# Optimization experiments

Hardware: AMD Instinct MI355X
Metric: run time of the kernel (lower is better)

Reference implementation:

```python
import jax, jax.numpy as jnp
import numpy as np

EPS_LN = 1e-5
EPS_STD = 1e-5


def _ln_dim1(z, g, b):
    # LayerNorm over channel dim (axis=1) of (B, C, T) or (B, C, 1)
    mu = z.mean(axis=1, keepdims=True)
    var = ((z - mu) ** 2).mean(axis=1, keepdims=True)
    return (z - mu) * jax.lax.rsqrt(var + EPS_LN) * g[None, :, None] + b[None, :, None]


def _stats(x, m):
    # weighted mean/std over time axis; m broadcasts over channels
    mean = (m * x).sum(axis=2)                                   # (B, C)
    std = jnp.sqrt(jnp.maximum((m * x * x).sum(axis=2) - mean ** 2, EPS_STD))
    return mean, std


def setup_inputs() -> dict:
    key = jax.random.key(0)
    ks = jax.random.split(key, 4)
    B, C, T, H = 16, 1536, 2000, 128
    x = jax.random.normal(ks[0], (B, C, T), dtype=jnp.float32)
    mask = jnp.ones((B, 1, T), dtype=jnp.float32)
    # attention MLP params (conv1x1 -> relu -> LN(dim=1) -> tanh -> conv1x1)
    w1 = jax.random.normal(ks[1], (H, 3 * C), dtype=jnp.float32) * (1.0 / np.sqrt(3 * C))
    b1 = jnp.zeros((H,), jnp.float32)
    g1 = jnp.ones((H,), jnp.float32)
    be1 = jnp.zeros((H,), jnp.float32)
    w2 = jax.random.normal(ks[2], (C, H), dtype=jnp.float32) * (1.0 / np.sqrt(H))
    b2 = jnp.zeros((C,), jnp.float32)
    g2 = jnp.ones((2 * C,), jnp.float32)
    be2 = jnp.zeros((2 * C,), jnp.float32)
    return {"x": x, "mask": mask, "w1": w1, "b1": b1, "g1": g1, "be1": be1,
            "w2": w2, "b2": b2, "g2": g2, "be2": be2}


def reference(x, mask, w1, b1, g1, be1, w2, b2, g2, be2):
    B, C, T = x.shape
    # time_attention: append masked global mean/std, broadcast over T
    total = mask.sum(axis=2, keepdims=True)                      # (B,1,1)
    mean0, std0 = _stats(x, mask / total)                        # (B,C)
    x_in = jnp.concatenate([
        x,
        jnp.broadcast_to(mean0[:, :, None], (B, C, T)),
        jnp.broadcast_to(std0[:, :, None], (B, C, T)),
    ], axis=1)                                                   # (B,3C,T)
    # attention MLP (conv1x1 == channel matmul)
    h = jnp.einsum("hc,bct->bht", w1, x_in) + b1[None, :, None]  # (B,H,T)
    h = jnp.tanh(_ln_dim1(jax.nn.relu(h), g1, be1))
    alpha = jnp.einsum("ch,bht->bct", w2, h) + b2[None, :, None]  # (B,C,T)
    # masked softmax over time
    alpha = jnp.where(mask == 0, -jnp.inf, alpha)
    alpha = jax.nn.softmax(alpha, axis=2)
    # attention-weighted stats
    mean, std = _stats(x, alpha)                                 # (B,C) each
    out = jnp.concatenate([mean, std], axis=1)[:, :, None]       # (B,2C,1)
    return _ln_dim1(out, g2, be2)
```

## Files before the change

### kernel.cpp

```cpp
#include <hip/hip_runtime.h>
#include <hip/hip_bf16.h>
#include <math.h>

constexpr int B_  = 16;
constexpr int C_  = 1536;
constexpr int T_  = 2000;
constexpr int H_  = 128;
constexpr int C3_ = 3 * C_;
constexpr int C2_ = 2 * C_;
constexpr int NT_ = 4;
constexpr int NTL_ = 32;
constexpr int KH_ = C_ / 2;

typedef short bf8 __attribute__((ext_vector_type(8)));
typedef short bf4 __attribute__((ext_vector_type(4)));
typedef float f4  __attribute__((ext_vector_type(4)));

__device__ inline unsigned short f2b(float f) {
  __bf16 h = (__bf16)f;
  return __builtin_bit_cast(unsigned short, h);
}

__global__ __launch_bounds__(256) void k_gemm1_stats(
    const float* __restrict__ x, const float* __restrict__ w1,
    const float* __restrict__ mask,
    float* __restrict__ h_pre, float* __restrict__ sp1, float* __restrict__ sp2) {
  __shared__ __align__(16) short As[2][128 * 32];
  __shared__ __align__(16) short Bs[2][64 * 32];
  const int b = blockIdx.y;
  const int tile = blockIdx.x;
  const int kbase = blockIdx.z * KH_;
  const int t0 = tile * 64;
  const int tid = threadIdx.x;
  const int lane = tid & 63;
  const int w = tid >> 6;
  const int l15 = lane & 15;
  const int l4 = lane >> 4;

  float4 va[4], vb[2];

  const int t4 = tid & 15;
  float mreg[4];
#pragma unroll
  for (int j = 0; j < 4; ++j) {
    int t = t0 + t4 * 4 + j;
    mreg[j] = (t < T_) ? mask[(size_t)b * T_ + t] : 0.f;
  }
  float* sp1row = sp1 + ((size_t)b * NTL_ + tile) * C_;
  float* sp2row = sp2 + ((size_t)b * NTL_ + tile) * C_;

  f4 acc[8];
#pragma unroll
  for (int mi = 0; mi < 8; ++mi) { f4 z = {0.f, 0.f, 0.f, 0.f}; acc[mi] = z; }

#define G1_GLOAD(K0)                                                          \
  {                                                                           \
    _Pragma("unroll")                                                         \
    for (int q = 0; q < 4; ++q) {                                             \
      int idx = q * 256 + tid;                                                \
      int row = idx >> 3, j4 = idx & 7;                                       \
      va[q] = *(const float4*)(w1 + (size_t)row * C3_ + (K0) + j4 * 4);       \
    }                                                                         \
    _Pragma("unroll")                                                         \
    for (int q = 0; q < 2; ++q) {                                             \
      int idx = q * 256 + tid;                                                \
      int k = idx >> 4;                                                       \
      int t = t0 + t4 * 4;                                                    \
      if (t < T_)                                                             \
        vb[q] = *(const float4*)(x + ((size_t)(b * C_ + (K0) + k)) * T_ + t); \
      else                                                                    \
        vb[q] = make_float4(0.f, 0.f, 0.f, 0.f);                              \
    }                                                                         \
  }
#define G1_LSTORE(BUF)                                                        \
  {                                                                           \
    _Pragma("unroll")                                                         \
    for (int q = 0; q < 4; ++q) {                                             \
      int idx = q * 256 + tid;                                                \
      int row = idx >> 3, j4 = idx & 7;                                       \
      int slot = (j4 >> 1) ^ ((row >> 2) & 3);                                \
      bf4 p;                                                                  \
      p[0] = (short)f2b(va[q].x); p[1] = (short)f2b(va[q].y);                 \
      p[2] = (short)f2b(va[q].z); p[3] = (short)f2b(va[q].w);                 \
      *(bf4*)&As[BUF][row * 32 + slot * 8 + (j4 & 1) * 4] = p;                \
    }                                                                         \
    _Pragma("unroll")                                                         \
    for (int q = 0; q < 2; ++q) {                                             \
      int idx = q * 256 + tid;                                                \
      int k = idx >> 4;                                                       \
      float vv[4] = {vb[q].x, vb[q].y, vb[q].z, vb[q].w};                     \
      _Pragma("unroll")                                                       \
      for (int j = 0; j < 4; ++j) {                                           \
        int row = t4 * 4 + j;                                                 \
        int slot = (k >> 3) ^ ((row >> 2) & 3);                               \
        Bs[BUF][row * 32 + slot * 8 + (k & 7)] = (short)f2b(vv[j]);           \
      }                                                                       \
    }                                                                         \
  }
#define G1_STATS(K0)                                                          \
  {                                                                           \
    _Pragma("unroll")                                                         \
    for (int q = 0; q < 2; ++q) {                                             \
      float vv[4] = {vb[q].x, vb[q].y, vb[q].z, vb[q].w};                     \
      float a1 = 0.f, a2 = 0.f;                                               \
      _Pragma("unroll")                                                       \
      for (int j = 0; j < 4; ++j) {                                           \
        float mx = mreg[j] * vv[j];                                           \
        a1 += mx;                                                             \
        a2 = fmaf(mx, vv[j], a2);                                             \
      }                                                                       \
      _Pragma("unroll")                                                       \
      for (int off = 1; off < 16; off <<= 1) {                                \
        a1 += __shfl_xor(a1, off);                                            \
        a2 += __shfl_xor(a2, off);                                            \
      }                                                                       \
      if (t4 == 0) {                                                          \
        int c = (K0) + q * 16 + (tid >> 4);                                   \
        sp1row[c] = a1;                                                       \
        sp2row[c] = a2;                                                       \
      }                                                                       \
    }                                                                         \
  }

  G1_GLOAD(kbase);
  G1_LSTORE(0);
  G1_STATS(kbase);
  __syncthreads();

  const int fA = (l15 >> 2) & 3;
  const int NS = KH_ / 32;
  for (int s = 0; s < NS; ++s) {
    const int cur = s & 1;
    if (s + 1 < NS) G1_GLOAD(kbase + (s + 1) * 32);
    {
      const int browB = w * 16 + l15;
      bf8 bfr = *(const bf8*)&Bs[cur][browB * 32 + (l4 ^ fA) * 8];
#pragma unroll
      for (int mi = 0; mi < 8; ++mi) {
        bf8 afr = *(const bf8*)&As[cur][(mi * 16 + l15) * 32 + (l4 ^ fA) * 8];
        acc[mi] = __builtin_amdgcn_mfma_f32_16x16x32_bf16(afr, bfr, acc[mi], 0, 0, 0);
      }
    }
    if (s + 1 < NS) {
      G1_LSTORE(cur ^ 1);
      G1_STATS(kbase + (s + 1) * 32);
    }
    __syncthreads();
  }

  const int t = t0 + w * 16 + l15;
  if (t < T_) {
    float* dst = h_pre + (size_t)blockIdx.z * B_ * T_ * H_ + ((size_t)b * T_ + t) * H_;
#pragma unroll
    for (int mi = 0; mi < 8; ++mi)
      *(f4*)&dst[mi * 16 + l4 * 4] = acc[mi];
  }
}

__global__ __launch_bounds__(256) void k_stats_reduce(
    const float* __restrict__ sp1, const float* __restrict__ sp2,
    const float* __restrict__ mask,
    float* __restrict__ mean0, float* __restrict__ std0) {
  __shared__ float rs[4];
  const int b = blockIdx.x / (C_ / 256);
  const int chunk = blockIdx.x % (C_ / 256);
  const int tid = threadIdx.x;
  const int lane = tid & 63;
  const int wv = tid >> 6;
  float sm = 0.f;
  for (int i = tid; i < T_; i += 256) sm += mask[(size_t)b * T_ + i];
#pragma unroll
  for (int off = 32; off; off >>= 1) sm += __shfl_xor(sm, off);
  if (lane == 0) rs[wv] = sm;
  __syncthreads();
  sm = rs[0] + rs[1] + rs[2] + rs[3];

  const int c = chunk * 256 + tid;
  float s1 = 0.f, s2 = 0.f;
#pragma unroll 8
  for (int tile = 0; tile < NTL_; ++tile) {
    const size_t j = ((size_t)b * NTL_ + tile) * C_ + c;
    s1 += sp1[j];
    s2 += sp2[j];
  }
  float mean = s1 / sm;
  float var = s2 / sm - mean * mean;
  mean0[b * C_ + c] = mean;
  std0[b * C_ + c] = sqrtf(fmaxf(var, 1e-5f));
}

__global__ __launch_bounds__(256) void k_hconst_wl1(
    const float* __restrict__ w1, const float* __restrict__ b1,
    const float* __restrict__ mean0, const float* __restrict__ std0,
    const float* __restrict__ w2,
    float* __restrict__ hconst, float* __restrict__ wl1) {
  const int wave = threadIdx.x >> 6;
  const int lane = threadIdx.x & 63;
  if (blockIdx.x < B_ * H_ / 4) {
    const int idx = blockIdx.x * 4 + wave;
    const int b = idx >> 7;
    const int h = idx & (H_ - 1);
    const float* wm  = w1 + (size_t)h * C3_ + C_;
    const float* wsd = wm + C_;
    const float* mn = mean0 + b * C_;
    const float* sd = std0 + b * C_;
    float s = 0.f;
    for (int c = lane; c < C_; c += 64)
      s += wm[c] * mn[c] + wsd[c] * sd[c];
#pragma unroll
    for (int off = 32; off; off >>= 1) s += __shfl_xor(s, off);
    if (lane == 0) hconst[idx] = s + b1[h];
  } else {
    const int c = (blockIdx.x - B_ * H_ / 4) * 4 + wave;
    const float* wr = w2 + (size_t)c * H_;
    float s = fabsf(wr[lane]) + fabsf(wr[lane + 64]);
#pragma unroll
    for (int off = 32; off; off >>= 1) s += __shfl_xor(s, off);
    if (lane == 0) wl1[c] = s;
  }
}

__global__ __launch_bounds__(256) void k_ln_epi(
    const float* __restrict__ h_pre, const float* __restrict__ hconst,
    const float* __restrict__ g1, const float* __restrict__ be1,
    unsigned short* __restrict__ hlnT) {
  const int b = blockIdx.y;
  const int t = blockIdx.x * 64 + (threadIdx.x >> 2);
  const int part = threadIdx.x & 3;
  if (t >= T_) return;
  const float* srcA = h_pre + ((size_t)b * T_ + t) * H_ + part * 32;
  const float* srcB = srcA + (size_t)B_ * T_ * H_;
  const float* hc = hconst + b * H_ + part * 32;
  float v[32];
  float sum = 0.f, ssq = 0.f;
#pragma unroll
  for (int j = 0; j < 8; ++j) {
    float4 hA = *(const float4*)(srcA + j * 4);
    float4 hB = *(const float4*)(srcB + j * 4);
    float4 c4 = *(const float4*)(hc + j * 4);
    const float* pa = (const float*)&hA;
    const float* pb = (const float*)&hB;
    const float* cp = (const float*)&c4;
#pragma unroll
    for (int r = 0; r < 4; ++r) {
      float u = fmaxf(pa[r] + pb[r] + cp[r], 0.f);
      v[j * 4 + r] = u;
      sum += u;
      ssq += u * u;
    }
  }
  sum += __shfl_xor(sum, 1); sum += __shfl_xor(sum, 2);
  ssq += __shfl_xor(ssq, 1); ssq += __shfl_xor(ssq, 2);
  const float mean = sum * (1.f / 128.f);
  const float rstd = rsqrtf(ssq * (1.f / 128.f) - mean * mean + 1e-5f);
  unsigned short* dst = hlnT + ((size_t)b * T_ + t) * H_ + part * 32;
  const float* gp = g1 + part * 32;
  const float* ep = be1 + part * 32;
#pragma unroll
  for (int m = 0; m < 4; ++m) {
    bf8 p;
#pragma unroll
    for (int r = 0; r < 8; ++r) {
      int j = m * 8 + r;
      p[r] = (short)f2b(tanhf((v[j] - mean) * rstd * gp[j] + ep[j]));
    }
    *(bf8*)&dst[m * 8] = p;
  }
}

__global__ __launch_bounds__(256) void k_gemm2_pool(
    const float* __restrict__ x, const float* __restrict__ mask,
    const float* __restrict__ w2, const unsigned short* __restrict__ hlnT,
    const float* __restrict__ wl1,
    float* __restrict__ ps0, float* __restrict__ ps1, float* __restrict__ ps2) {
  __shared__ __align__(16) short Hs[2][64 * 128];
  const int b = blockIdx.y;
  const int c0 = blockIdx.x * 64;
  const int part = blockIdx.z;
  const int tb = part * 512;
  const int te = min(tb + 512, T_);
  const int tid = threadIdx.x;
  const int lane = tid & 63;
  const int w = tid >> 6;
  const int l15 = lane & 15;
  const int l4 = lane >> 4;

  bf8 af[4];
#pragma unroll
  for (int ks = 0; ks < 4; ++ks) {
    const float* src = w2 + (size_t)(c0 + w * 16 + l15) * H_ + (ks * 4 + l4) * 8;
    float4 v0 = *(const float4*)src;
    float4 v1 = *(const float4*)(src + 4);
    bf8 p;
    p[0] = (short)f2b(v0.x); p[1] = (short)f2b(v0.y);
    p[2] = (short)f2b(v0.z); p[3] = (short)f2b(v0.w);
    p[4] = (short)f2b(v1.x); p[5] = (short)f2b(v1.y);
    p[6] = (short)f2b(v1.z); p[7] = (short)f2b(v1.w);
    af[ks] = p;
  }

  float Mc[4];
  {
    float4 m4 = *(const float4*)(wl1 + c0 + w * 16 + l4 * 4);
    Mc[0] = m4.x; Mc[1] = m4.y; Mc[2] = m4.z; Mc[3] = m4.w;
  }

  float s0[4], s1[4], s2[4];
#pragma unroll
  for (int r = 0; r < 4; ++r) { s0[r] = 0.f; s1[r] = 0.f; s2[r] = 0.f; }

  bf8 hreg[4];
#define G2_HLOAD(T0)                                                          \
  {                                                                           \
    _Pragma("unroll")                                                         \
    for (int q = 0; q < 4; ++q) {                                             \
      int idx = q * 256 + tid;                                                \
      int row = idx >> 4, slot = idx & 15;                                    \
      int t = (T0) + row;                                                     \
      if (t > T_ - 1) t = T_ - 1;                                             \
      hreg[q] = *(const bf8*)(hlnT + ((size_t)b * T_ + t) * H_ + slot * 8);   \
    }                                                                         \
  }
#define G2_HSTORE(BUF)                                                        \
  {                                                                           \
    _Pragma("unroll")                                                         \
    for (int q = 0; q < 4; ++q) {                                             \
      int idx = q * 256 + tid;                                                \
      int row = idx >> 4, slot = idx & 15;                                    \
      *(bf8*)&Hs[BUF][row * 128 + (slot ^ (row & 15)) * 8] = hreg[q];         \
    }                                                                         \
  }

  G2_HLOAD(tb);
  G2_HSTORE(0);
  __syncthreads();

  const int NCH = (te - tb + 63) / 64;
  for (int ch = 0; ch < NCH; ++ch) {
    const int t0 = tb + ch * 64;
    const int cur = ch & 1;
    if (ch + 1 < NCH) G2_HLOAD(t0 + 64);

    float mk[4];
    int tcol[4];
#pragma unroll
    for (int nj = 0; nj < 4; ++nj) {
      int t = t0 + nj * 16 + l15;
      tcol[nj] = (t < T_) ? t : (T_ - 1);
      mk[nj] = (t < T_) ? mask[(size_t)b * T_ + t] : 0.f;
    }
    float xv[4][4];
#pragma unroll
    for (int reg = 0; reg < 4; ++reg) {
      const int c = c0 + w * 16 + l4 * 4 + reg;
      const float* xrow = x + ((size_t)(b * C_ + c)) * T_;
#pragma unroll
      for (int nj = 0; nj < 4; ++nj) xv[reg][nj] = xrow[tcol[nj]];
    }

    f4 acc[4];
#pragma unroll
    for (int nj = 0; nj < 4; ++nj) { f4 z = {0.f, 0.f, 0.f, 0.f}; acc[nj] = z; }

#pragma unroll
    for (int ks = 0; ks < 4; ++ks) {
      const int sw = (ks * 4 + l4) ^ l15;
      bf8 bb[4];
#pragma unroll
      for (int nj = 0; nj < 4; ++nj)
        bb[nj] = *(const bf8*)&Hs[cur][(nj * 16 + l15) * 128 + sw * 8];
#pragma unroll
      for (int nj = 0; nj < 4; ++nj)
        acc[nj] = __builtin_amdgcn_mfma_f32_16x16x32_bf16(af[ks], bb[nj], acc[nj], 0, 0, 0);
    }

#pragma unroll
    for (int reg = 0; reg < 4; ++reg) {
      float a0 = s0[reg], a1 = s1[reg], a2 = s2[reg];
#pragma unroll
      for (int nj = 0; nj < 4; ++nj) {
        float e = (mk[nj] != 0.f) ? __expf(acc[nj][reg] - Mc[reg]) : 0.f;
        float xvv = xv[reg][nj];
        a0 += e; a1 += e * xvv; a2 += e * xvv * xvv;
      }
      s0[reg] = a0; s1[reg] = a1; s2[reg] = a2;
    }

    if (ch + 1 < NCH) G2_HSTORE(cur ^ 1);
    __syncthreads();
  }

#pragma unroll
  for (int off = 1; off < 16; off <<= 1) {
#pragma unroll
    for (int r = 0; r < 4; ++r) {
      s0[r] += __shfl_xor(s0[r], off);
      s1[r] += __shfl_xor(s1[r], off);
      s2[r] += __shfl_xor(s2[r], off);
    }
  }
  if (l15 == 0) {
#pragma unroll
    for (int reg = 0; reg < 4; ++reg) {
      const int c = c0 + w * 16 + l4 * 4 + reg;
      const size_t j = ((size_t)(b * NT_ + part)) * C_ + c;
      ps0[j] = s0[reg]; ps1[j] = s1[reg]; ps2[j] = s2[reg];
    }
  }
}

__global__ __launch_bounds__(256) void k_pool_merge(
    const float* __restrict__ ps0, const float* __restrict__ ps1,
    const float* __restrict__ ps2, float* __restrict__ pooled) {
  const int idx = blockIdx.x * 256 + threadIdx.x;
  const int b = idx / C_;
  const int c = idx - b * C_;
  float s0 = 0.f, s1 = 0.f, s2 = 0.f;
#pragma unroll
  for (int p = 0; p < NT_; ++p) {
    const size_t j = ((size_t)(b * NT_ + p)) * C_ + c;
    s0 += ps0[j]; s1 += ps1[j]; s2 += ps2[j];
  }
  float mean = s1 / s0;
  float var = s2 / s0 - mean * mean;
  pooled[b * C2_ + c] = mean;
  pooled[b * C2_ + C_ + c] = sqrtf(fmaxf(var, 1e-5f));
}

__global__ __launch_bounds__(256) void k_final_ln(
    const float* __restrict__ pooled, const float* __restrict__ g2,
    const float* __restrict__ be2, float* __restrict__ out) {
  __shared__ float rs[8];
  const int b = blockIdx.x;
  const int tid = threadIdx.x;
  const int lane = tid & 63;
  const int wave = tid >> 6;
  const float* p = pooled + b * C2_;
  float s = 0.f, q = 0.f;
  for (int i = tid; i < C2_; i += 256) {
    float v = p[i];
    s += v;
    q += v * v;
  }
#pragma unroll
  for (int off = 32; off; off >>= 1) {
    s += __shfl_xor(s, off);
    q += __shfl_xor(q, off);
  }
  if (lane == 0) { rs[wave] = s; rs[4 + wave] = q; }
  __syncthreads();
  s = rs[0] + rs[1] + rs[2] + rs[3];
  q = rs[4] + rs[5] + rs[6] + rs[7];
  float mean = s * (1.f / C2_);
  float var = q * (1.f / C2_) - mean * mean;
  float rstd = rsqrtf(var + 1e-5f);
  for (int i = tid; i < C2_; i += 256)
    out[b * C2_ + i] = (p[i] - mean) * rstd * g2[i] + be2[i];
}

extern "C" void kernel_launch(void* const* d_in, const int* in_sizes, int n_in,
                              void* d_out, int out_size, void* d_ws, size_t ws_size,
                              hipStream_t stream) {
  const float* x    = (const float*)d_in[0];
  const float* mask = (const float*)d_in[1];
  const float* w1   = (const float*)d_in[2];
  const float* b1   = (const float*)d_in[3];
  const float* g1   = (const float*)d_in[4];
  const float* be1  = (const float*)d_in[5];
  const float* w2   = (const float*)d_in[6];
  const float* g2   = (const float*)d_in[8];
  const float* be2  = (const float*)d_in[9];
  float* out = (float*)d_out;

  float* ws     = (float*)d_ws;
  float* mean0  = ws;
  float* std0   = mean0 + B_ * C_;
  float* hconst = std0 + B_ * C_;
  float* pooled = hconst + B_ * H_;
  float* wl1    = pooled + B_ * C2_;
  float* ps0    = wl1 + C_;
  float* ps1    = ps0 + B_ * NT_ * C_;
  float* ps2    = ps1 + B_ * NT_ * C_;
  float* sp1    = ps2 + B_ * NT_ * C_;
  float* sp2    = sp1 + B_ * NTL_ * C_;
  float* h_pre  = sp2 + B_ * NTL_ * C_;
  unsigned short* hlnT = (unsigned short*)(h_pre + 2 * (size_t)B_ * T_ * H_);

  k_gemm1_stats<<<dim3(NTL_, B_, 2), dim3(256), 0, stream>>>(x, w1, mask, h_pre, sp1, sp2);
  k_stats_reduce<<<dim3(B_ * C_ / 256), dim3(256), 0, stream>>>(sp1, sp2, mask, mean0, std0);
  k_hconst_wl1<<<dim3(B_ * H_ / 4 + C_ / 4), dim3(256), 0, stream>>>(
      w1, b1, mean0, std0, w2, hconst, wl1);
  k_ln_epi<<<dim3(NTL_, B_), dim3(256), 0, stream>>>(h_pre, hconst, g1, be1, hlnT);
  k_gemm2_pool<<<dim3(C_ / 64, B_, NT_), dim3(256), 0, stream>>>(x, mask, w2, hlnT, wl1,
                                                                 ps0, ps1, ps2);
  k_pool_merge<<<dim3(B_ * C_ / 256), dim3(256), 0, stream>>>(ps0, ps1, ps2, pooled);
  k_final_ln<<<dim3(B_), dim3(256), 0, stream>>>(pooled, g2, be2, out);
}
```

Measured before the change: 161.2 us.

## Interleave standalone stats blocks into GEMM1 launch and drop stats reduce kernel

Replaces the per-tile partial-stats computation inside the GEMM1 loop and the separate reduction kernel with dedicated stats blocks launched in the same grid (6 stats blocks per GEMM block), each wave computing masked mean/std for one channel row directly. Also changes the x tile load to per-thread column gathers of 8 rows, written as a single bf8 LDS store instead of scattered 16-bit stores. This removes a kernel launch and the sp1/sp2 partial buffers, and shortens the GEMM inner loop. The cost is that x is read twice from global memory (once by the stats blocks, once by the GEMM blocks), and the new x loads are strided across rows.

```diff
diff --git a/kernel.cpp b/kernel.cpp
--- a/kernel.cpp
+++ b/kernel.cpp
@@ -11,6 +11,8 @@
 constexpr int NT_ = 4;
 constexpr int NTL_ = 32;
 constexpr int KH_ = C_ / 2;
+constexpr int NG1_ = NTL_ * B_ * 2;
+constexpr int NST_ = B_ * C_ / 4;
 
 typedef short bf8 __attribute__((ext_vector_type(8)));
 typedef short bf4 __attribute__((ext_vector_type(4)));
@@ -21,33 +23,60 @@
   return __builtin_bit_cast(unsigned short, h);
 }
 
-__global__ __launch_bounds__(256) void k_gemm1_stats(
+__global__ __launch_bounds__(256) void k_g1_and_stats(
     const float* __restrict__ x, const float* __restrict__ w1,
     const float* __restrict__ mask,
-    float* __restrict__ h_pre, float* __restrict__ sp1, float* __restrict__ sp2) {
+    float* __restrict__ h_pre, float* __restrict__ mean0, float* __restrict__ std0) {
   __shared__ __align__(16) short As[2][128 * 32];
   __shared__ __align__(16) short Bs[2][64 * 32];
-  const int b = blockIdx.y;
-  const int tile = blockIdx.x;
-  const int kbase = blockIdx.z * KH_;
+  const int tid = threadIdx.x;
+  const int gid = blockIdx.x / 7;
+  const int rem = blockIdx.x % 7;
+
+  if (rem != 0) {
+    const int sid = gid * 6 + rem - 1;
+    const int wave = tid >> 6;
+    const int lane = tid & 63;
+    const int row = sid * 4 + wave;
+    const int b = row / C_;
+    const float4* xr = (const float4*)(x + (size_t)row * T_);
+    const float4* mr = (const float4*)(mask + (size_t)b * T_);
+    float sm = 0.f, s1 = 0.f, s2 = 0.f;
+    for (int i = lane; i < T_ / 4; i += 64) {
+      float4 xv = xr[i];
+      float4 mv = mr[i];
+      sm += mv.x + mv.y + mv.z + mv.w;
+      s1 += mv.x * xv.x + mv.y * xv.y + mv.z * xv.z + mv.w * xv.w;
+      s2 += mv.x * xv.x * xv.x + mv.y * xv.y * xv.y + mv.z * xv.z * xv.z + mv.w * xv.w * xv.w;
+    }
+#pragma unroll
+    for (int off = 32; off; off >>= 1) {
+      sm += __shfl_xor(sm, off);
+      s1 += __shfl_xor(s1, off);
+      s2 += __shfl_xor(s2, off);
+    }
+    if (lane == 0) {
+      float mean = s1 / sm;
+      float var = s2 / sm - mean * mean;
+      mean0[row] = mean;
+      std0[row] = sqrtf(fmaxf(var, 1e-5f));
+    }
+    return;
+  }
+
+  const int tile = gid & 31;
+  const int b = (gid >> 5) & 15;
+  const int kbase = (gid >> 9) * KH_;
   const int t0 = tile * 64;
-  const int tid = threadIdx.x;
   const int lane = tid & 63;
   const int w = tid >> 6;
   const int l15 = lane & 15;
   const int l4 = lane >> 4;
-
-  float4 va[4], vb[2];
-
-  const int t4 = tid & 15;
-  float mreg[4];
-#pragma unroll
-  for (int j = 0; j < 4; ++j) {
-    int t = t0 + t4 * 4 + j;
-    mreg[j] = (t < T_) ? mask[(size_t)b * T_ + t] : 0.f;
-  }
-  float* sp1row = sp1 + ((size_t)b * NTL_ + tile) * C_;
-  float* sp2row = sp2 + ((size_t)b * NTL_ + tile) * C_;
+  const int tl = tid & 63;
+  const int kq = tid >> 6;
+
+  float4 va[4];
+  float xs[8];
 
   f4 acc[8];
 #pragma unroll
@@ -61,15 +90,16 @@
       int row = idx >> 3, j4 = idx & 7;                                       \
       va[q] = *(const float4*)(w1 + (size_t)row * C3_ + (K0) + j4 * 4);       \
     }                                                                         \
-    _Pragma("unroll")                                                         \
-    for (int q = 0; q < 2; ++q) {                                             \
-      int idx = q * 256 + tid;                                                \
-      int k = idx >> 4;                                                       \
-      int t = t0 + t4 * 4;                                                    \
-      if (t < T_)                                                             \
-        vb[q] = *(const float4*)(x + ((size_t)(b * C_ + (K0) + k)) * T_ + t); \
-      else                                                                    \
-        vb[q] = make_float4(0.f, 0.f, 0.f, 0.f);                              \
+    {                                                                         \
+      int t = t0 + tl;                                                        \
+      const float* xb = x + ((size_t)(b * C_ + (K0) + kq * 8)) * T_ + t;      \
+      if (t < T_) {                                                           \
+        _Pragma("unroll")                                                     \
+        for (int j = 0; j < 8; ++j) xs[j] = xb[(size_t)j * T_];               \
+      } else {                                                                \
+        _Pragma("unroll")                                                     \
+        for (int j = 0; j < 8; ++j) xs[j] = 0.f;                              \
+      }                                                                       \
     }                                                                         \
   }
 #define G1_LSTORE(BUF)                                                        \
@@ -84,47 +114,16 @@
       p[2] = (short)f2b(va[q].z); p[3] = (short)f2b(va[q].w);                 \
       *(bf4*)&As[BUF][row * 32 + slot * 8 + (j4 & 1) * 4] = p;                \
     }                                                                         \
-    _Pragma("unroll")                                                         \
-    for (int q = 0; q < 2; ++q) {                                             \
-      int idx = q * 256 + tid;                                                \
-      int k = idx >> 4;                                                       \
-      float vv[4] = {vb[q].x, vb[q].y, vb[q].z, vb[q].w};                     \
+    {                                                                         \
+      bf8 p;                                                                  \
       _Pragma("unroll")                                                       \
-      for (int j = 0; j < 4; ++j) {                                           \
-        int row = t4 * 4 + j;                                                 \
-        int slot = (k >> 3) ^ ((row >> 2) & 3);                               \
-        Bs[BUF][row * 32 + slot * 8 + (k & 7)] = (short)f2b(vv[j]);           \
-      }                                                                       \
-    }                                                                         \
-  }
-#define G1_STATS(K0)                                                          \
-  {                                                                           \
-    _Pragma("unroll")                                                         \
-    for (int q = 0; q < 2; ++q) {                                             \
-      float vv[4] = {vb[q].x, vb[q].y, vb[q].z, vb[q].w};                     \
-      float a1 = 0.f, a2 = 0.f;                                               \
-      _Pragma("unroll")                                                       \
-      for (int j = 0; j < 4; ++j) {                                           \
-        float mx = mreg[j] * vv[j];                                           \
-        a1 += mx;                                                             \
-        a2 = fmaf(mx, vv[j], a2);                                             \
-      }                                                                       \
-      _Pragma("unroll")                                                       \
-      for (int off = 1; off < 16; off <<= 1) {                                \
-        a1 += __shfl_xor(a1, off);                                            \
-        a2 += __shfl_xor(a2, off);                                            \
-      }                                                                       \
-      if (t4 == 0) {                                                          \
-        int c = (K0) + q * 16 + (tid >> 4);                                   \
-        sp1row[c] = a1;                                                       \
-        sp2row[c] = a2;                                                       \
-      }                                                                       \
+      for (int j = 0; j < 8; ++j) p[j] = (short)f2b(xs[j]);                   \
+      *(bf8*)&Bs[BUF][tl * 32 + (kq ^ ((tl >> 2) & 3)) * 8] = p;              \
     }                                                                         \
   }
 
   G1_GLOAD(kbase);
   G1_LSTORE(0);
-  G1_STATS(kbase);
   __syncthreads();
 
   const int fA = (l15 >> 2) & 3;
@@ -141,52 +140,17 @@
         acc[mi] = __builtin_amdgcn_mfma_f32_16x16x32_bf16(afr, bfr, acc[mi], 0, 0, 0);
       }
     }
-    if (s + 1 < NS) {
-      G1_LSTORE(cur ^ 1);
-      G1_STATS(kbase + (s + 1) * 32);
-    }
+    if (s + 1 < NS) G1_LSTORE(cur ^ 1);
     __syncthreads();
   }
 
   const int t = t0 + w * 16 + l15;
   if (t < T_) {
-    float* dst = h_pre + (size_t)blockIdx.z * B_ * T_ * H_ + ((size_t)b * T_ + t) * H_;
+    float* dst = h_pre + (size_t)(gid >> 9) * B_ * T_ * H_ + ((size_t)b * T_ + t) * H_;
 #pragma unroll
     for (int mi = 0; mi < 8; ++mi)
       *(f4*)&dst[mi * 16 + l4 * 4] = acc[mi];
   }
-}
-
-__global__ __launch_bounds__(256) void k_stats_reduce(
-    const float* __restrict__ sp1, const float* __restrict__ sp2,
-    const float* __restrict__ mask,
-    float* __restrict__ mean0, float* __restrict__ std0) {
-  __shared__ float rs[4];
-  const int b = blockIdx.x / (C_ / 256);
-  const int chunk = blockIdx.x % (C_ / 256);
-  const int tid = threadIdx.x;
-  const int lane = tid & 63;
-  const int wv = tid >> 6;
-  float sm = 0.f;
-  for (int i = tid; i < T_; i += 256) sm += mask[(size_t)b * T_ + i];
-#pragma unroll
-  for (int off = 32; off; off >>= 1) sm += __shfl_xor(sm, off);
-  if (lane == 0) rs[wv] = sm;
-  __syncthreads();
-  sm = rs[0] + rs[1] + rs[2] + rs[3];
-
-  const int c = chunk * 256 + tid;
-  float s1 = 0.f, s2 = 0.f;
-#pragma unroll 8
-  for (int tile = 0; tile < NTL_; ++tile) {
-    const size_t j = ((size_t)b * NTL_ + tile) * C_ + c;
-    s1 += sp1[j];
-    s2 += sp2[j];
-  }
-  float mean = s1 / sm;
-  float var = s2 / sm - mean * mean;
-  mean0[b * C_ + c] = mean;
-  std0[b * C_ + c] = sqrtf(fmaxf(var, 1e-5f));
 }
 
 __global__ __launch_bounds__(256) void k_hconst_wl1(
@@ -481,13 +445,10 @@
   float* ps0    = wl1 + C_;
   float* ps1    = ps0 + B_ * NT_ * C_;
   float* ps2    = ps1 + B_ * NT_ * C_;
-  float* sp1    = ps2 + B_ * NT_ * C_;
-  float* sp2    = sp1 + B_ * NTL_ * C_;
-  float* h_pre  = sp2 + B_ * NTL_ * C_;
+  float* h_pre  = ps2 + B_ * NT_ * C_;
   unsigned short* hlnT = (unsigned short*)(h_pre + 2 * (size_t)B_ * T_ * H_);
 
-  k_gemm1_stats<<<dim3(NTL_, B_, 2), dim3(256), 0, stream>>>(x, w1, mask, h_pre, sp1, sp2);
-  k_stats_reduce<<<dim3(B_ * C_ / 256), dim3(256), 0, stream>>>(sp1, sp2, mask, mean0, std0);
+  k_g1_and_stats<<<dim3(7 * NG1_), dim3(256), 0, stream>>>(x, w1, mask, h_pre, mean0, std0);
   k_hconst_wl1<<<dim3(B_ * H_ / 4 + C_ / 4), dim3(256), 0, stream>>>(
       w1, b1, mean0, std0, w2, hconst, wl1);
   k_ln_epi<<<dim3(NTL_, B_), dim3(256), 0, stream>>>(h_pre, hconst, g1, be1, hlnT);
```

Result: slower. 175.4 us (+8.8%).
